# Kernel tuning notes

Hardware: AMD Instinct MI355X
Metric: run time of the kernel (lower is better)

Reference implementation:

```python
import jax, jax.numpy as jnp
import numpy as np

BASIS_SIZE = 256          # levels of the bitfield code
R_MAX = 1.0               # quantization range for normalized weights
QMAX = BASIS_SIZE // 2 - 1  # 127 -> symmetric int8-style grid
EPS = 1e-8


def setup_inputs() -> dict:
    key = jax.random.key(0)
    kx, kw, kb = jax.random.split(key, 3)
    B, S, D_IN, D_OUT = 4, 2048, 4096, 4096
    x = jax.random.normal(kx, (B, S, D_IN), dtype=jnp.float32)
    W = jax.random.normal(kw, (D_OUT, D_IN), dtype=jnp.float32)
    bias = jax.random.normal(kb, (D_OUT,), dtype=jnp.float32)
    return {"x": x, "W": W, "bias": bias}


def _bitfield_dequant_weight(W):
    # per-output-row L2 norm (p=2, dim=1 in torch)
    weight_norms = jnp.sqrt(jnp.sum(W * W, axis=1))          # [out]
    W_normalized = W / (weight_norms[:, None] + EPS)          # rows ~unit norm
    # bitfield encode/decode: uniform symmetric quantization to BASIS_SIZE
    # levels in [-R_MAX, R_MAX]
    scale = R_MAX / QMAX
    Wq = jnp.round(jnp.clip(W_normalized, -R_MAX, R_MAX) / scale) * scale
    return Wq, weight_norms


def reference(x, W, bias):
    Wq, weight_norms = _bitfield_dequant_weight(W)
    B, S, D_IN = x.shape
    x2 = x.reshape(-1, D_IN)                                  # [B*S, in]
    # bitfield matmul on normalized weights
    out_norm = jnp.einsum('nd,od->no', x2, Wq)                # [B*S, out]
    # denormalize (restore row norms) + bias epilogue
    out = out_norm * weight_norms
    out = out.reshape(B, S, -1) + bias
    return out
```

## Files before the change

### kernel.cpp

```cpp
#include <hip/hip_runtime.h>

typedef __attribute__((ext_vector_type(4))) int i32x4;
typedef __attribute__((ext_vector_type(16))) int i32x16;
typedef __attribute__((address_space(3))) char lds3;

#define D_IN  4096
#define D_OUT 4096
#define M_TOT 8192

__device__ __forceinline__ void async16(const void* g, lds3* l) {
  __builtin_amdgcn_global_load_lds(
      (__attribute__((address_space(1))) void*)g,
      (__attribute__((address_space(3))) void*)l,
      16, 0, 0);
}

#define DSR(dst, addr, off) \
  asm volatile("ds_read_b128 %0, %1 offset:%2" : "=v"(dst) : "v"(addr), "i"(off))

__device__ __forceinline__ int pack4(float a, float b, float c, float d, float s) {
  int q0 = (int)rintf(a * s) & 255;
  int q1 = (int)rintf(b * s) & 255;
  int q2 = (int)rintf(c * s) & 255;
  int q3 = (int)rintf(d * s) & 255;
  return q0 | (q1 << 8) | (q2 << 16) | (q3 << 24);
}

__global__ void quant_x_kernel(const float* __restrict__ x, int* __restrict__ xq,
                               float* __restrict__ sx) {
  const int row = blockIdx.x * 4 + (threadIdx.x >> 6);
  const int lane = threadIdx.x & 63;
  const float4* xr = (const float4*)(x + (size_t)row * D_IN);

  float4 v[16];
  float mx = 0.f;
#pragma unroll
  for (int j = 0; j < 16; j++) {
    v[j] = xr[j * 64 + lane];
    mx = fmaxf(mx, fmaxf(fmaxf(fabsf(v[j].x), fabsf(v[j].y)),
                         fmaxf(fabsf(v[j].z), fabsf(v[j].w))));
  }
#pragma unroll
  for (int off = 32; off; off >>= 1) mx = fmaxf(mx, __shfl_xor(mx, off));
  if (lane == 0) sx[row] = mx * (1.0f / 127.0f);

  const float inv = 127.0f / mx;
  int* xqr = xq + (size_t)row * (D_IN / 4);
#pragma unroll
  for (int j = 0; j < 16; j++)
    xqr[j * 64 + lane] = pack4(v[j].x, v[j].y, v[j].z, v[j].w, inv);
}

__global__ void quant_w_kernel(const float* __restrict__ W, int* __restrict__ wq,
                               float* __restrict__ sn) {
  const int row = blockIdx.x * 4 + (threadIdx.x >> 6);
  const int lane = threadIdx.x & 63;
  const float4* wr = (const float4*)(W + (size_t)row * D_IN);

  float4 v[16];
  double ss = 0.0;
#pragma unroll
  for (int j = 0; j < 16; j++) {
    v[j] = wr[j * 64 + lane];
    ss += (double)v[j].x * v[j].x + (double)v[j].y * v[j].y +
          (double)v[j].z * v[j].z + (double)v[j].w * v[j].w;
  }
#pragma unroll
  for (int off = 32; off; off >>= 1) ss += __shfl_xor(ss, off);
  const float nrm = (float)sqrt(ss);
  if (lane == 0) sn[row] = nrm * (1.0f / 127.0f);

  const float den = nrm + 1e-8f;
  int* wqr = wq + (size_t)row * (D_IN / 4);
#pragma unroll
  for (int j = 0; j < 16; j++) {
    float e[4] = {v[j].x, v[j].y, v[j].z, v[j].w};
    int q[4];
#pragma unroll
    for (int c = 0; c < 4; c++) {
      float wn = e[c] / den;
      wn = fminf(1.0f, fmaxf(-1.0f, wn));
      q[c] = (int)rintf(wn * 127.0f) & 255;
    }
    wqr[j * 64 + lane] = q[0] | (q[1] << 8) | (q[2] << 16) | (q[3] << 24);
  }
}

template<int BUF, int VM, bool ISSA, bool ISSB>
__device__ __forceinline__ void ktile(const unsigned (&aAk)[4], const unsigned (&aBk)[4],
                                      const char* pA, const char* pB,
                                      lds3* lA, lds3* lB,
                                      i32x4 (&af)[2][4], i32x4 (&bf)[8],
                                      i32x16 (&acc)[4][2]) {
  constexpr int AB = BUF * 32768;
  constexpr int OB = (BUF ^ 1) * 32768;

  DSR(bf[0], aBk[0], AB + 0);
  DSR(bf[1], aBk[1], AB + 0);
  DSR(bf[2], aBk[2], AB + 0);
  DSR(bf[3], aBk[3], AB + 0);
  DSR(bf[4], aBk[0], AB + 4096);
  DSR(bf[5], aBk[1], AB + 4096);
  DSR(bf[6], aBk[2], AB + 4096);
  DSR(bf[7], aBk[3], AB + 4096);
  DSR(af[0][0], aAk[0], AB + 0);
  DSR(af[0][1], aAk[1], AB + 0);
  DSR(af[0][2], aAk[2], AB + 0);
  DSR(af[0][3], aAk[3], AB + 0);
  if (ISSA) { async16(pA, lA + OB);
              async16(pA + (size_t)64 * D_IN, lA + OB + 8192); }
  asm volatile("s_barrier" ::: "memory");
  asm volatile("s_waitcnt lgkmcnt(0)"
               : "+v"(af[0][0]), "+v"(af[0][1]), "+v"(af[0][2]), "+v"(af[0][3]),
                 "+v"(bf[0]), "+v"(bf[1]), "+v"(bf[2]), "+v"(bf[3]),
                 "+v"(bf[4]), "+v"(bf[5]), "+v"(bf[6]), "+v"(bf[7]));
  __builtin_amdgcn_sched_barrier(0);
  __builtin_amdgcn_s_setprio(1);
#pragma unroll
  for (int kk = 0; kk < 4; kk++) {
    acc[0][0] = __builtin_amdgcn_mfma_i32_32x32x32_i8(af[0][kk], bf[kk],     acc[0][0], 0, 0, 0);
    acc[0][1] = __builtin_amdgcn_mfma_i32_32x32x32_i8(af[0][kk], bf[4 + kk], acc[0][1], 0, 0, 0);
  }
  __builtin_amdgcn_s_setprio(0);
  __builtin_amdgcn_sched_barrier(0);
  asm volatile("s_barrier" ::: "memory");

  DSR(af[1][0], aAk[0], AB + 4096);
  DSR(af[1][1], aAk[1], AB + 4096);
  DSR(af[1][2], aAk[2], AB + 4096);
  DSR(af[1][3], aAk[3], AB + 4096);
  if (ISSA) { async16(pA + (size_t)128 * D_IN, lA + OB + 16384);
              async16(pA + (size_t)192 * D_IN, lA + OB + 24576); }
  asm volatile("s_barrier" ::: "memory");
  asm volatile("s_waitcnt lgkmcnt(0)"
               : "+v"(af[1][0]), "+v"(af[1][1]), "+v"(af[1][2]), "+v"(af[1][3]));
  __builtin_amdgcn_sched_barrier(0);
  __builtin_amdgcn_s_setprio(1);
#pragma unroll
  for (int kk = 0; kk < 4; kk++) {
    acc[1][0] = __builtin_amdgcn_mfma_i32_32x32x32_i8(af[1][kk], bf[kk],     acc[1][0], 0, 0, 0);
    acc[1][1] = __builtin_amdgcn_mfma_i32_32x32x32_i8(af[1][kk], bf[4 + kk], acc[1][1], 0, 0, 0);
  }
  __builtin_amdgcn_s_setprio(0);
  __builtin_amdgcn_sched_barrier(0);
  asm volatile("s_barrier" ::: "memory");

  DSR(af[0][0], aAk[0], AB + 8192);
  DSR(af[0][1], aAk[1], AB + 8192);
  DSR(af[0][2], aAk[2], AB + 8192);
  DSR(af[0][3], aAk[3], AB + 8192);
  if (ISSB) { async16(pB, lB + AB);
              async16(pB + (size_t)64 * D_IN, lB + AB + 8192); }
  asm volatile("s_barrier" ::: "memory");
  asm volatile("s_waitcnt lgkmcnt(0)"
               : "+v"(af[0][0]), "+v"(af[0][1]), "+v"(af[0][2]), "+v"(af[0][3]));
  __builtin_amdgcn_sched_barrier(0);
  __builtin_amdgcn_s_setprio(1);
#pragma unroll
  for (int kk = 0; kk < 4; kk++) {
    acc[2][0] = __builtin_amdgcn_mfma_i32_32x32x32_i8(af[0][kk], bf[kk],     acc[2][0], 0, 0, 0);
    acc[2][1] = __builtin_amdgcn_mfma_i32_32x32x32_i8(af[0][kk], bf[4 + kk], acc[2][1], 0, 0, 0);
  }
  __builtin_amdgcn_s_setprio(0);
  __builtin_amdgcn_sched_barrier(0);
  asm volatile("s_barrier" ::: "memory");

  DSR(af[1][0], aAk[0], AB + 12288);
  DSR(af[1][1], aAk[1], AB + 12288);
  DSR(af[1][2], aAk[2], AB + 12288);
  DSR(af[1][3], aAk[3], AB + 12288);
  if (ISSB) { async16(pB + (size_t)128 * D_IN, lB + AB + 16384);
              async16(pB + (size_t)192 * D_IN, lB + AB + 24576); }
  asm volatile("s_barrier" ::: "memory");
  asm volatile("s_waitcnt lgkmcnt(0)"
               : "+v"(af[1][0]), "+v"(af[1][1]), "+v"(af[1][2]), "+v"(af[1][3]));
  __builtin_amdgcn_sched_barrier(0);
  __builtin_amdgcn_s_setprio(1);
#pragma unroll
  for (int kk = 0; kk < 4; kk++) {
    acc[3][0] = __builtin_amdgcn_mfma_i32_32x32x32_i8(af[1][kk], bf[kk],     acc[3][0], 0, 0, 0);
    acc[3][1] = __builtin_amdgcn_mfma_i32_32x32x32_i8(af[1][kk], bf[4 + kk], acc[3][1], 0, 0, 0);
  }
  __builtin_amdgcn_s_setprio(0);
  __builtin_amdgcn_sched_barrier(0);
  asm volatile("s_waitcnt vmcnt(%0)" :: "i"(VM));
  asm volatile("s_barrier" ::: "memory");
}

__global__ __launch_bounds__(512, 2)
void gemm_i8_kernel(const char* __restrict__ A, const char* __restrict__ B,
                    const float* __restrict__ sx, const float* __restrict__ sn,
                    const float* __restrict__ bias, float* __restrict__ C) {
  __shared__ __align__(16) char smem[131072];

  const int t = threadIdx.x;
  const int lane = t & 63;
  const int wave = t >> 6;
  const int wm = wave >> 2, wn = wave & 3;

  const int bid = blockIdx.x;
  const int swz = ((bid & 7) << 6) | (bid >> 3);
  const int m0 = (swz >> 4) * 256;
  const int n0 = (swz & 15) * 256;

  const int srow = t >> 3;
  const int sch  = (t & 7) ^ (srow & 7);
  const char* gA = A + (size_t)(m0 + srow) * D_IN + sch * 16;
  const char* gB = B + (size_t)(n0 + srow) * D_IN + sch * 16;
  lds3* l3 = (lds3*)smem;
  lds3* lA = l3 + t * 16;
  lds3* lB = l3 + 65536 + t * 16;

  const int l31 = lane & 31;
  const int hi  = lane >> 5;
  const int e   = lane & 7;
  const unsigned base = (unsigned)(size_t)l3;
  unsigned aAk[4], aBk[4];
#pragma unroll
  for (int kk = 0; kk < 4; kk++) {
    const unsigned sw = (unsigned)(((kk * 2 + hi) ^ e) << 4);
    aAk[kk] = base + (wm * 128 + l31) * 128 + sw;
    aBk[kk] = base + 65536 + (wn * 64 + l31) * 128 + sw;
  }

  i32x16 acc[4][2];
#pragma unroll
  for (int i = 0; i < 4; i++)
#pragma unroll
    for (int j = 0; j < 2; j++) acc[i][j] = (i32x16)0;
  i32x4 af[2][4], bf[8];

  async16(gB,                       lB);
  async16(gB + (size_t)64  * D_IN,  lB + 8192);
  async16(gB + (size_t)128 * D_IN,  lB + 16384);
  async16(gB + (size_t)192 * D_IN,  lB + 24576);
  async16(gA,                       lA);
  async16(gA + (size_t)64  * D_IN,  lA + 8192);
  async16(gA + (size_t)128 * D_IN,  lA + 16384);
  async16(gA + (size_t)192 * D_IN,  lA + 24576);
  async16(gB + 128,                      lB + 32768);
  async16(gB + 128 + (size_t)64  * D_IN, lB + 32768 + 8192);
  async16(gB + 128 + (size_t)128 * D_IN, lB + 32768 + 16384);
  async16(gB + 128 + (size_t)192 * D_IN, lB + 32768 + 24576);
  asm volatile("s_waitcnt vmcnt(4)");
  asm volatile("s_barrier" ::: "memory");

  const char* pA = gA + 128;
  const char* pB = gB + 256;

#pragma unroll 1
  for (int it = 0; it < 15; ++it) {
    ktile<0, 4, true, true>(aAk, aBk, pA, pB, lA, lB, af, bf, acc); pA += 128; pB += 128;
    ktile<1, 4, true, true>(aAk, aBk, pA, pB, lA, lB, af, bf, acc); pA += 128; pB += 128;
  }
  ktile<0, 0, true,  false>(aAk, aBk, pA, pB, lA, lB, af, bf, acc); pA += 128;
  ktile<1, 0, false, false>(aAk, aBk, pA, pB, lA, lB, af, bf, acc);

#pragma unroll
  for (int mi = 0; mi < 4; mi++) {
    const int rb = m0 + wm * 128 + mi * 32 + hi * 4;
    float sxv[16];
#pragma unroll
    for (int r = 0; r < 16; r++) sxv[r] = sx[rb + (r & 3) + 8 * (r >> 2)];
#pragma unroll
    for (int ni = 0; ni < 2; ni++) {
      const int col = n0 + wn * 64 + ni * 32 + l31;
      const float scn = sn[col];
      const float bv  = bias[col];
#pragma unroll
      for (int r = 0; r < 16; r++) {
        const int row = rb + (r & 3) + 8 * (r >> 2);
        C[(size_t)row * D_OUT + col] =
            (float)acc[mi][ni][r] * (sxv[r] * scn) + bv;
      }
    }
  }
}

extern "C" void kernel_launch(void* const* d_in, const int* in_sizes, int n_in,
                              void* d_out, int out_size, void* d_ws, size_t ws_size,
                              hipStream_t stream) {
  const float* x    = (const float*)d_in[0];
  const float* W    = (const float*)d_in[1];
  const float* bias = (const float*)d_in[2];
  float* out = (float*)d_out;

  char* ws = (char*)d_ws;
  char*  xq = ws;
  char*  wq = ws + (size_t)M_TOT * D_IN;
  float* sx = (float*)(wq + (size_t)D_OUT * D_IN);
  float* sn = sx + M_TOT;

  quant_x_kernel<<<M_TOT / 4, 256, 0, stream>>>(x, (int*)xq, sx);
  quant_w_kernel<<<D_OUT / 4, 256, 0, stream>>>(W, (int*)wq, sn);
  gemm_i8_kernel<<<512, 512, 0, stream>>>(xq, wq, sx, sn, bias, out);
}
```

Measured before the change: 399.5 us.

## Restructure int8 GEMM to 4 waves with 4-stage K=64 LDS pipeline

Reworks the GEMM main loop from 8 waves with 128x64 per-wave tiles and a double-buffered K=128 pipeline to 4 waves with 128x128 per-wave tiles and a 4-stage ring of K=64 slices. It uses a new LDS swizzle for 64-byte rows and issues both A and B loads three stages ahead. Fragment reads for the second half of each slice are overlapped with the MFMAs of the first half, and there is one barrier per slice instead of several. The aim is fewer barriers and more operand reuse per LDS read. In exchange each wave needs many more accumulator registers, and occupancy drops to one 256-thread block.

```diff
diff --git a/kernel.cpp b/kernel.cpp
--- a/kernel.cpp
+++ b/kernel.cpp
@@ -86,108 +86,65 @@
   }
 }
 
-template<int BUF, int VM, bool ISSA, bool ISSB>
-__device__ __forceinline__ void ktile(const unsigned (&aAk)[4], const unsigned (&aBk)[4],
+#define MFMA16(F, acc) \
+  _Pragma("unroll") \
+  for (int mi = 0; mi < 4; mi++) \
+    _Pragma("unroll") \
+    for (int ni = 0; ni < 4; ni++) \
+      acc[mi][ni] = __builtin_amdgcn_mfma_i32_32x32x32_i8(F[mi], F[4 + ni], acc[mi][ni], 0, 0, 0);
+
+template<int S, int VM, bool ISSUE, bool SYNC>
+__device__ __forceinline__ void ktile(unsigned aA0, unsigned aA1,
+                                      unsigned aB0, unsigned aB1,
                                       const char* pA, const char* pB,
                                       lds3* lA, lds3* lB,
-                                      i32x4 (&af)[2][4], i32x4 (&bf)[8],
-                                      i32x16 (&acc)[4][2]) {
-  constexpr int AB = BUF * 32768;
-  constexpr int OB = (BUF ^ 1) * 32768;
-
-  DSR(bf[0], aBk[0], AB + 0);
-  DSR(bf[1], aBk[1], AB + 0);
-  DSR(bf[2], aBk[2], AB + 0);
-  DSR(bf[3], aBk[3], AB + 0);
-  DSR(bf[4], aBk[0], AB + 4096);
-  DSR(bf[5], aBk[1], AB + 4096);
-  DSR(bf[6], aBk[2], AB + 4096);
-  DSR(bf[7], aBk[3], AB + 4096);
-  DSR(af[0][0], aAk[0], AB + 0);
-  DSR(af[0][1], aAk[1], AB + 0);
-  DSR(af[0][2], aAk[2], AB + 0);
-  DSR(af[0][3], aAk[3], AB + 0);
-  if (ISSA) { async16(pA, lA + OB);
-              async16(pA + (size_t)64 * D_IN, lA + OB + 8192); }
-  asm volatile("s_barrier" ::: "memory");
+                                      i32x4 (&f0)[8], i32x4 (&f1)[8],
+                                      i32x16 (&acc)[4][4]) {
+  const unsigned tA0 = aA0 + S * 32768, tA1 = aA1 + S * 32768;
+  const unsigned tB0 = aB0 + S * 32768, tB1 = aB1 + S * 32768;
+
+  DSR(f0[0], tA0, 0);  DSR(f0[1], tA0, 2048);  DSR(f0[2], tA0, 4096);  DSR(f0[3], tA0, 6144);
+  DSR(f0[4], tB0, 0);  DSR(f0[5], tB0, 2048);  DSR(f0[6], tB0, 4096);  DSR(f0[7], tB0, 6144);
+
+  if (ISSUE) {
+    constexpr int T = ((S + 3) & 3) * 32768;
+    async16(pA,                          lA + T);
+    async16(pA + (size_t)64  * D_IN,     lA + T + 4096);
+    async16(pA + (size_t)128 * D_IN,     lA + T + 8192);
+    async16(pA + (size_t)192 * D_IN,     lA + T + 12288);
+    async16(pB,                          lB + T);
+    async16(pB + (size_t)64  * D_IN,     lB + T + 4096);
+    async16(pB + (size_t)128 * D_IN,     lB + T + 8192);
+    async16(pB + (size_t)192 * D_IN,     lB + T + 12288);
+  }
+
   asm volatile("s_waitcnt lgkmcnt(0)"
-               : "+v"(af[0][0]), "+v"(af[0][1]), "+v"(af[0][2]), "+v"(af[0][3]),
-                 "+v"(bf[0]), "+v"(bf[1]), "+v"(bf[2]), "+v"(bf[3]),
-                 "+v"(bf[4]), "+v"(bf[5]), "+v"(bf[6]), "+v"(bf[7]));
-  __builtin_amdgcn_sched_barrier(0);
-  __builtin_amdgcn_s_setprio(1);
-#pragma unroll
-  for (int kk = 0; kk < 4; kk++) {
-    acc[0][0] = __builtin_amdgcn_mfma_i32_32x32x32_i8(af[0][kk], bf[kk],     acc[0][0], 0, 0, 0);
-    acc[0][1] = __builtin_amdgcn_mfma_i32_32x32x32_i8(af[0][kk], bf[4 + kk], acc[0][1], 0, 0, 0);
-  }
-  __builtin_amdgcn_s_setprio(0);
-  __builtin_amdgcn_sched_barrier(0);
-  asm volatile("s_barrier" ::: "memory");
-
-  DSR(af[1][0], aAk[0], AB + 4096);
-  DSR(af[1][1], aAk[1], AB + 4096);
-  DSR(af[1][2], aAk[2], AB + 4096);
-  DSR(af[1][3], aAk[3], AB + 4096);
-  if (ISSA) { async16(pA + (size_t)128 * D_IN, lA + OB + 16384);
-              async16(pA + (size_t)192 * D_IN, lA + OB + 24576); }
-  asm volatile("s_barrier" ::: "memory");
+               : "+v"(f0[0]), "+v"(f0[1]), "+v"(f0[2]), "+v"(f0[3]),
+                 "+v"(f0[4]), "+v"(f0[5]), "+v"(f0[6]), "+v"(f0[7]));
+  __builtin_amdgcn_sched_barrier(0);
+
+  DSR(f1[0], tA1, 0);  DSR(f1[1], tA1, 2048);  DSR(f1[2], tA1, 4096);  DSR(f1[3], tA1, 6144);
+  DSR(f1[4], tB1, 0);  DSR(f1[5], tB1, 2048);  DSR(f1[6], tB1, 4096);  DSR(f1[7], tB1, 6144);
+  __builtin_amdgcn_sched_barrier(0);
+
+  MFMA16(f0, acc);
+  __builtin_amdgcn_sched_barrier(0);
+
   asm volatile("s_waitcnt lgkmcnt(0)"
-               : "+v"(af[1][0]), "+v"(af[1][1]), "+v"(af[1][2]), "+v"(af[1][3]));
-  __builtin_amdgcn_sched_barrier(0);
-  __builtin_amdgcn_s_setprio(1);
-#pragma unroll
-  for (int kk = 0; kk < 4; kk++) {
-    acc[1][0] = __builtin_amdgcn_mfma_i32_32x32x32_i8(af[1][kk], bf[kk],     acc[1][0], 0, 0, 0);
-    acc[1][1] = __builtin_amdgcn_mfma_i32_32x32x32_i8(af[1][kk], bf[4 + kk], acc[1][1], 0, 0, 0);
-  }
-  __builtin_amdgcn_s_setprio(0);
-  __builtin_amdgcn_sched_barrier(0);
-  asm volatile("s_barrier" ::: "memory");
-
-  DSR(af[0][0], aAk[0], AB + 8192);
-  DSR(af[0][1], aAk[1], AB + 8192);
-  DSR(af[0][2], aAk[2], AB + 8192);
-  DSR(af[0][3], aAk[3], AB + 8192);
-  if (ISSB) { async16(pB, lB + AB);
-              async16(pB + (size_t)64 * D_IN, lB + AB + 8192); }
-  asm volatile("s_barrier" ::: "memory");
-  asm volatile("s_waitcnt lgkmcnt(0)"
-               : "+v"(af[0][0]), "+v"(af[0][1]), "+v"(af[0][2]), "+v"(af[0][3]));
-  __builtin_amdgcn_sched_barrier(0);
-  __builtin_amdgcn_s_setprio(1);
-#pragma unroll
-  for (int kk = 0; kk < 4; kk++) {
-    acc[2][0] = __builtin_amdgcn_mfma_i32_32x32x32_i8(af[0][kk], bf[kk],     acc[2][0], 0, 0, 0);
-    acc[2][1] = __builtin_amdgcn_mfma_i32_32x32x32_i8(af[0][kk], bf[4 + kk], acc[2][1], 0, 0, 0);
-  }
-  __builtin_amdgcn_s_setprio(0);
-  __builtin_amdgcn_sched_barrier(0);
-  asm volatile("s_barrier" ::: "memory");
-
-  DSR(af[1][0], aAk[0], AB + 12288);
-  DSR(af[1][1], aAk[1], AB + 12288);
-  DSR(af[1][2], aAk[2], AB + 12288);
-  DSR(af[1][3], aAk[3], AB + 12288);
-  if (ISSB) { async16(pB + (size_t)128 * D_IN, lB + AB + 16384);
-              async16(pB + (size_t)192 * D_IN, lB + AB + 24576); }
-  asm volatile("s_barrier" ::: "memory");
-  asm volatile("s_waitcnt lgkmcnt(0)"
-               : "+v"(af[1][0]), "+v"(af[1][1]), "+v"(af[1][2]), "+v"(af[1][3]));
-  __builtin_amdgcn_sched_barrier(0);
-  __builtin_amdgcn_s_setprio(1);
-#pragma unroll
-  for (int kk = 0; kk < 4; kk++) {
-    acc[3][0] = __builtin_amdgcn_mfma_i32_32x32x32_i8(af[1][kk], bf[kk],     acc[3][0], 0, 0, 0);
-    acc[3][1] = __builtin_amdgcn_mfma_i32_32x32x32_i8(af[1][kk], bf[4 + kk], acc[3][1], 0, 0, 0);
-  }
-  __builtin_amdgcn_s_setprio(0);
-  __builtin_amdgcn_sched_barrier(0);
-  asm volatile("s_waitcnt vmcnt(%0)" :: "i"(VM));
-  asm volatile("s_barrier" ::: "memory");
-}
-
-__global__ __launch_bounds__(512, 2)
+               : "+v"(f1[0]), "+v"(f1[1]), "+v"(f1[2]), "+v"(f1[3]),
+                 "+v"(f1[4]), "+v"(f1[5]), "+v"(f1[6]), "+v"(f1[7]));
+  __builtin_amdgcn_sched_barrier(0);
+
+  MFMA16(f1, acc);
+
+  if (SYNC) {
+    __builtin_amdgcn_sched_barrier(0);
+    asm volatile("s_waitcnt vmcnt(%0)" :: "i"(VM));
+    asm volatile("s_barrier" ::: "memory");
+  }
+}
+
+__global__ __launch_bounds__(256, 1)
 void gemm_i8_kernel(const char* __restrict__ A, const char* __restrict__ B,
                     const float* __restrict__ sx, const float* __restrict__ sn,
                     const float* __restrict__ bias, float* __restrict__ C) {
@@ -196,65 +153,67 @@
   const int t = threadIdx.x;
   const int lane = t & 63;
   const int wave = t >> 6;
-  const int wm = wave >> 2, wn = wave & 3;
+  const int wm = wave >> 1, wn = wave & 1;
 
   const int bid = blockIdx.x;
   const int swz = ((bid & 7) << 6) | (bid >> 3);
   const int m0 = (swz >> 4) * 256;
   const int n0 = (swz & 15) * 256;
 
-  const int srow = t >> 3;
-  const int sch  = (t & 7) ^ (srow & 7);
+  const int srow = t >> 2;
+  const int sch  = (t & 3) ^ ((t >> 3) & 3);
   const char* gA = A + (size_t)(m0 + srow) * D_IN + sch * 16;
   const char* gB = B + (size_t)(n0 + srow) * D_IN + sch * 16;
   lds3* l3 = (lds3*)smem;
   lds3* lA = l3 + t * 16;
-  lds3* lB = l3 + 65536 + t * 16;
+  lds3* lB = l3 + 16384 + t * 16;
 
   const int l31 = lane & 31;
   const int hi  = lane >> 5;
-  const int e   = lane & 7;
+  const int s3  = (l31 >> 1) & 3;
   const unsigned base = (unsigned)(size_t)l3;
-  unsigned aAk[4], aBk[4];
-#pragma unroll
-  for (int kk = 0; kk < 4; kk++) {
-    const unsigned sw = (unsigned)(((kk * 2 + hi) ^ e) << 4);
-    aAk[kk] = base + (wm * 128 + l31) * 128 + sw;
-    aBk[kk] = base + 65536 + (wn * 64 + l31) * 128 + sw;
-  }
-
-  i32x16 acc[4][2];
+  const unsigned aA0 = base + (wm * 128 + l31) * 64 + (unsigned)(((0 + hi) ^ s3) << 4);
+  const unsigned aA1 = base + (wm * 128 + l31) * 64 + (unsigned)(((2 + hi) ^ s3) << 4);
+  const unsigned aB0 = base + 16384 + (wn * 128 + l31) * 64 + (unsigned)(((0 + hi) ^ s3) << 4);
+  const unsigned aB1 = base + 16384 + (wn * 128 + l31) * 64 + (unsigned)(((2 + hi) ^ s3) << 4);
+
+  i32x16 acc[4][4];
 #pragma unroll
   for (int i = 0; i < 4; i++)
 #pragma unroll
-    for (int j = 0; j < 2; j++) acc[i][j] = (i32x16)0;
-  i32x4 af[2][4], bf[8];
-
-  async16(gB,                       lB);
-  async16(gB + (size_t)64  * D_IN,  lB + 8192);
-  async16(gB + (size_t)128 * D_IN,  lB + 16384);
-  async16(gB + (size_t)192 * D_IN,  lB + 24576);
-  async16(gA,                       lA);
-  async16(gA + (size_t)64  * D_IN,  lA + 8192);
-  async16(gA + (size_t)128 * D_IN,  lA + 16384);
-  async16(gA + (size_t)192 * D_IN,  lA + 24576);
-  async16(gB + 128,                      lB + 32768);
-  async16(gB + 128 + (size_t)64  * D_IN, lB + 32768 + 8192);
-  async16(gB + 128 + (size_t)128 * D_IN, lB + 32768 + 16384);
-  async16(gB + 128 + (size_t)192 * D_IN, lB + 32768 + 24576);
-  asm volatile("s_waitcnt vmcnt(4)");
+    for (int j = 0; j < 4; j++) acc[i][j] = (i32x16)0;
+  i32x4 f0[8], f1[8];
+
+#pragma unroll
+  for (int s = 0; s < 3; s++) {
+    const char* qA = gA + s * 64;
+    const char* qB = gB + s * 64;
+    async16(qA,                      lA + s * 32768);
+    async16(qA + (size_t)64  * D_IN, lA + s * 32768 + 4096);
+    async16(qA + (size_t)128 * D_IN, lA + s * 32768 + 8192);
+    async16(qA + (size_t)192 * D_IN, lA + s * 32768 + 12288);
+    async16(qB,                      lB + s * 32768);
+    async16(qB + (size_t)64  * D_IN, lB + s * 32768 + 4096);
+    async16(qB + (size_t)128 * D_IN, lB + s * 32768 + 8192);
+    async16(qB + (size_t)192 * D_IN, lB + s * 32768 + 12288);
+  }
+  asm volatile("s_waitcnt vmcnt(16)");
   asm volatile("s_barrier" ::: "memory");
 
-  const char* pA = gA + 128;
-  const char* pB = gB + 256;
+  const char* pA = gA + 3 * 64;
+  const char* pB = gB + 3 * 64;
 
 #pragma unroll 1
   for (int it = 0; it < 15; ++it) {
-    ktile<0, 4, true, true>(aAk, aBk, pA, pB, lA, lB, af, bf, acc); pA += 128; pB += 128;
-    ktile<1, 4, true, true>(aAk, aBk, pA, pB, lA, lB, af, bf, acc); pA += 128; pB += 128;
-  }
-  ktile<0, 0, true,  false>(aAk, aBk, pA, pB, lA, lB, af, bf, acc); pA += 128;
-  ktile<1, 0, false, false>(aAk, aBk, pA, pB, lA, lB, af, bf, acc);
+    ktile<0, 16, true, true>(aA0, aA1, aB0, aB1, pA, pB, lA, lB, f0, f1, acc); pA += 64; pB += 64;
+    ktile<1, 16, true, true>(aA0, aA1, aB0, aB1, pA, pB, lA, lB, f0, f1, acc); pA += 64; pB += 64;
+    ktile<2, 16, true, true>(aA0, aA1, aB0, aB1, pA, pB, lA, lB, f0, f1, acc); pA += 64; pB += 64;
+    ktile<3, 16, true, true>(aA0, aA1, aB0, aB1, pA, pB, lA, lB, f0, f1, acc); pA += 64; pB += 64;
+  }
+  ktile<0, 16, true,  true >(aA0, aA1, aB0, aB1, pA, pB, lA, lB, f0, f1, acc);
+  ktile<1,  8, false, true >(aA0, aA1, aB0, aB1, pA, pB, lA, lB, f0, f1, acc);
+  ktile<2,  0, false, true >(aA0, aA1, aB0, aB1, pA, pB, lA, lB, f0, f1, acc);
+  ktile<3,  0, false, false>(aA0, aA1, aB0, aB1, pA, pB, lA, lB, f0, f1, acc);
 
 #pragma unroll
   for (int mi = 0; mi < 4; mi++) {
@@ -263,8 +222,8 @@
 #pragma unroll
     for (int r = 0; r < 16; r++) sxv[r] = sx[rb + (r & 3) + 8 * (r >> 2)];
 #pragma unroll
-    for (int ni = 0; ni < 2; ni++) {
-      const int col = n0 + wn * 64 + ni * 32 + l31;
+    for (int ni = 0; ni < 4; ni++) {
+      const int col = n0 + wn * 128 + ni * 32 + l31;
       const float scn = sn[col];
       const float bv  = bias[col];
 #pragma unroll
@@ -293,5 +252,5 @@
 
   quant_x_kernel<<<M_TOT / 4, 256, 0, stream>>>(x, (int*)xq, sx);
   quant_w_kernel<<<D_OUT / 4, 256, 0, stream>>>(W, (int*)wq, sn);
-  gemm_i8_kernel<<<512, 512, 0, stream>>>(xq, wq, sx, sn, bias, out);
-}
+  gemm_i8_kernel<<<512, 256, 0, stream>>>(xq, wq, sx, sn, bias, out);
+}
```

After: 400.7 us. About the same (+0.3%).
